# Performance work log

Hardware: AMD Instinct MI355X
Metric: run time of the kernel (lower is better)

Reference implementation:

```python
import jax, jax.numpy as jnp
import numpy as np

N = 100000        # num nodes
E = 1200000       # num edges (avg degree 12)
F_IN = 64         # num_features
HID = 64          # hidden_size
NCLS = 40         # num_classes
K = 2             # propagation hops


def setup_inputs() -> dict:
    key = jax.random.key(0)
    k0, k1, k2, k3 = jax.random.split(key, 4)
    x = jax.random.normal(k0, (N, F_IN), dtype=jnp.float32)
    edge_index = jax.random.randint(k1, (2, E), 0, N, dtype=jnp.int32)
    # SGConv's internal Linear (in->hidden) and the classifier fc (hidden->classes)
    W1 = jax.random.normal(k2, (F_IN, HID), dtype=jnp.float32) / np.sqrt(F_IN).astype(np.float32)
    b1 = jnp.zeros((HID,), jnp.float32)
    W2 = jax.random.normal(k3, (HID, NCLS), dtype=jnp.float32) / np.sqrt(HID).astype(np.float32)
    b2 = jnp.zeros((NCLS,), jnp.float32)
    return {"x": x, "edge_index": edge_index, "W1": W1, "b1": b1, "W2": W2, "b2": b2}


def reference(x, edge_index, W1, b1, W2, b2):
    n = x.shape[0]
    # gcn_norm: add self-loops with weight 1, symmetric normalization
    loop = jnp.arange(n, dtype=edge_index.dtype)
    src = jnp.concatenate([edge_index[0], loop])  # message source j
    dst = jnp.concatenate([edge_index[1], loop])  # aggregation target i
    deg = jax.ops.segment_sum(jnp.ones(src.shape, x.dtype), dst, num_segments=n)
    dinv = jnp.where(deg > 0, jax.lax.rsqrt(deg), 0.0)
    norm = dinv[src] * dinv[dst]  # [E+N]
    # K-hop propagation: x_i <- sum_j norm_ij * x_j
    for _ in range(K):
        x = jax.ops.segment_sum(norm[:, None] * x[src], dst, num_segments=n)
    h = jax.nn.relu(x @ W1 + b1)          # SGConv lin + ReLU
    logits = h @ W2 + b2                  # fc
    return jax.nn.log_softmax(logits, axis=1)
```

## Files before the change

kernel.cpp:

```cpp
#include <hip/hip_runtime.h>
#include <math.h>

#define N_NODES 100000
#define BSHIFT 9
#define NBUCK 256

typedef unsigned short bfu;
typedef unsigned int uint;
typedef __attribute__((ext_vector_type(8))) short short8v;
typedef __attribute__((ext_vector_type(4))) float f32x4;

__device__ __forceinline__ float bf2f(bfu u) {
    union { uint i; float f; } v; v.i = (uint)u << 16; return v.f;
}
__device__ __forceinline__ bfu f2bf(float f) {
    union { float f_; uint i; } v; v.f_ = f;
    uint r = (v.i + 0x7FFFu + ((v.i >> 16) & 1u)) >> 16;
    return (bfu)r;
}

__global__ __launch_bounds__(256) void bucket_hist(const int* __restrict__ dst,
                                                   int* __restrict__ gcount, int nE) {
    __shared__ int h[NBUCK];
    int tid = threadIdx.x;
    h[tid] = 0;
    __syncthreads();
    for (int e = blockIdx.x * 256 + tid; e < nE; e += gridDim.x * 256)
        atomicAdd(&h[dst[e] >> BSHIFT], 1);
    __syncthreads();
    if (h[tid]) atomicAdd(&gcount[tid], h[tid]);
}

__global__ __launch_bounds__(NBUCK) void scan_buckets(const int* __restrict__ gcount,
                                                      int* __restrict__ gbase,
                                                      int* __restrict__ gcursor) {
    __shared__ int s[NBUCK];
    int t = threadIdx.x;
    int v = gcount[t];
    s[t] = v;
    __syncthreads();
    #pragma unroll
    for (int off = 1; off < NBUCK; off <<= 1) {
        int tv = (t >= off) ? s[t - off] : 0;
        __syncthreads();
        s[t] += tv;
        __syncthreads();
    }
    gbase[t] = s[t] - v;
    gcursor[t] = s[t] - v;
}

__global__ __launch_bounds__(256) void bin_edges(const int* __restrict__ src,
                                                 const int* __restrict__ dst,
                                                 int* __restrict__ gcursor,
                                                 uint* __restrict__ binned, int nE) {
    __shared__ int h[NBUCK];
    __shared__ int base[NBUCK];
    int tid = threadIdx.x;
    int start = blockIdx.x * 4096;
    h[tid] = 0;
    __syncthreads();
    int bkt[16], rnk[16];
    #pragma unroll
    for (int u = 0; u < 16; ++u) {
        int e = start + u * 256 + tid;
        bkt[u] = -1;
        if (e < nE) {
            int b = dst[e] >> BSHIFT;
            bkt[u] = b;
            rnk[u] = atomicAdd(&h[b], 1);
        }
    }
    __syncthreads();
    base[tid] = h[tid] ? atomicAdd(&gcursor[tid], h[tid]) : 0;
    __syncthreads();
    #pragma unroll
    for (int u = 0; u < 16; ++u) {
        int e = start + u * 256 + tid;
        if (e < nE) {
            uint pk = ((uint)(dst[e] & 511) << 17) | (uint)src[e];
            binned[base[bkt[u]] + rnk[u]] = pk;
        }
    }
}

__global__ __launch_bounds__(512) void build_csr(
    const uint* __restrict__ binned, const int* __restrict__ gbase,
    const int* __restrict__ gcount, int* __restrict__ rowptr,
    float* __restrict__ dinv, int* __restrict__ nbr, int nN, int nE) {
    __shared__ int hist[512];
    __shared__ int cursor[512];
    int b = blockIdx.x, t = threadIdx.x;
    int n0 = b << BSHIFT;
    int nNodes = min(512, nN - n0);
    int base = gbase[b], cnt = gcount[b];
    hist[t] = 0;
    __syncthreads();
    for (int i = t; i < cnt; i += 512)
        atomicAdd(&hist[binned[base + i] >> 17], 1);
    __syncthreads();
    int v = hist[t];
    #pragma unroll
    for (int off = 1; off < 512; off <<= 1) {
        int tv = (t >= off) ? hist[t - off] : 0;
        __syncthreads();
        hist[t] += tv;
        __syncthreads();
    }
    int excl = hist[t] - v;
    if (t < nNodes) {
        rowptr[n0 + t] = base + excl;
        dinv[n0 + t] = rsqrtf((float)v + 1.0f);
    }
    cursor[t] = excl;
    __syncthreads();
    for (int i = t; i < cnt; i += 512) {
        uint pk = binned[base + i];
        int ld = pk >> 17;
        int pos = atomicAdd(&cursor[ld], 1);
        nbr[base + pos] = (int)(pk & 0x1FFFFu);
    }
    if (b == 0 && t == 0) rowptr[nN] = nE;
}

__global__ void scale_to_bf16(ushort4* __restrict__ z0, const float4* __restrict__ x,
                              const float* __restrict__ dinv, int n4) {
    int t = blockIdx.x * blockDim.x + threadIdx.x;
    if (t >= n4) return;
    float w = dinv[t >> 4];
    float4 v = x[t];
    ushort4 o;
    o.x = f2bf(w * v.x); o.y = f2bf(w * v.y);
    o.z = f2bf(w * v.z); o.w = f2bf(w * v.w);
    z0[t] = o;
}

template<int PW>
__global__ __launch_bounds__(256) void gather_hop8(
    bfu* __restrict__ out, const bfu* __restrict__ z,
    const int* __restrict__ nbr, const int* __restrict__ rowptr,
    const float* __restrict__ dinv, int nN) {
    int node = blockIdx.x * 4 + (threadIdx.x >> 6);
    if (node >= nN) return;
    int lane = threadIdx.x & 63;
    int g = lane >> 3, k = lane & 7;
    int beg = rowptr[node], end = rowptr[node + 1];

    float acc[8];
    #pragma unroll
    for (int i = 0; i < 8; ++i) acc[i] = 0.f;

    auto accum = [&](uint4 v) {
        union { uint u; float f; } t;
        t.u = v.x << 16;         acc[0] += t.f;
        t.u = v.x & 0xFFFF0000u; acc[1] += t.f;
        t.u = v.y << 16;         acc[2] += t.f;
        t.u = v.y & 0xFFFF0000u; acc[3] += t.f;
        t.u = v.z << 16;         acc[4] += t.f;
        t.u = v.z & 0xFFFF0000u; acc[5] += t.f;
        t.u = v.w << 16;         acc[6] += t.f;
        t.u = v.w & 0xFFFF0000u; acc[7] += t.f;
    };

    if (g == 0)
        accum(reinterpret_cast<const uint4*>(z + (size_t)node * 64)[k]);
    for (int j = beg + g; j < end; j += 8)
        accum(reinterpret_cast<const uint4*>(z + (size_t)nbr[j] * 64)[k]);

    #pragma unroll
    for (int m = 8; m < 64; m <<= 1)
        #pragma unroll
        for (int i = 0; i < 8; ++i)
            acc[i] += __shfl_xor(acc[i], m);

    if (g == 0) {
        float di = dinv[node];
        float w = (PW == 2) ? di * di : di;
        uint4 o;
        o.x = ((uint)f2bf(acc[1] * w) << 16) | f2bf(acc[0] * w);
        o.y = ((uint)f2bf(acc[3] * w) << 16) | f2bf(acc[2] * w);
        o.z = ((uint)f2bf(acc[5] * w) << 16) | f2bf(acc[4] * w);
        o.w = ((uint)f2bf(acc[7] * w) << 16) | f2bf(acc[6] * w);
        reinterpret_cast<uint4*>(out + (size_t)node * 64)[k] = o;
    }
}

__global__ __launch_bounds__(256) void mlp_mfma(
    float* __restrict__ out, const bfu* __restrict__ zC,
    const float* __restrict__ W1, const float* __restrict__ b1,
    const float* __restrict__ W2, const float* __restrict__ b2, int nN) {
    __shared__ short w1t[64 * 72];
    __shared__ short w2t[48 * 72];
    __shared__ short hlds[64 * 72];
    __shared__ float b1s[64];
    __shared__ float b2s[48];

    int tid = threadIdx.x;
    for (int i = tid; i < 64 * 64; i += 256) {
        int k = i >> 6, n = i & 63;
        w1t[n * 72 + k] = (short)f2bf(W1[i]);
    }
    for (int i = tid; i < 48 * 64; i += 256) {
        int k = i / 48, n = i % 48;
        w2t[n * 72 + k] = (short)(n < 40 ? f2bf(W2[k * 40 + n]) : 0);
    }
    if (tid < 64) b1s[tid] = b1[tid];
    if (tid >= 64 && tid < 112) b2s[tid - 64] = (tid - 64 < 40) ? b2[tid - 64] : 0.f;

    int wv = tid >> 6, l = tid & 63;
    int li = l & 15, kg = l >> 4;
    int nodebase = blockIdx.x * 64 + wv * 16;
    int nclamp = min(nodebase + li, nN - 1);

    const short8v* zr = (const short8v*)(zC + (size_t)nclamp * 64);
    short8v a0 = zr[kg];
    short8v a1 = zr[kg + 4];
    __syncthreads();

    f32x4 acc[4];
    #pragma unroll
    for (int nt = 0; nt < 4; ++nt) {
        f32x4 c = {0.f, 0.f, 0.f, 0.f};
        short8v b0 = *(const short8v*)&w1t[(nt * 16 + li) * 72 + kg * 8];
        short8v b1f = *(const short8v*)&w1t[(nt * 16 + li) * 72 + 32 + kg * 8];
        c = __builtin_amdgcn_mfma_f32_16x16x32_bf16(a0, b0, c, 0, 0, 0);
        c = __builtin_amdgcn_mfma_f32_16x16x32_bf16(a1, b1f, c, 0, 0, 0);
        acc[nt] = c;
    }
    #pragma unroll
    for (int nt = 0; nt < 4; ++nt) {
        float bb = b1s[nt * 16 + li];
        #pragma unroll
        for (int r = 0; r < 4; ++r) {
            float v = fmaxf(acc[nt][r] + bb, 0.f);
            hlds[(wv * 16 + kg * 4 + r) * 72 + nt * 16 + li] = (short)f2bf(v);
        }
    }
    __syncthreads();

    const short8v* hp = (const short8v*)&hlds[(wv * 16 + li) * 72];
    short8v ha0 = hp[kg];
    short8v ha1 = hp[kg + 4];
    f32x4 acc2[3];
    #pragma unroll
    for (int nt = 0; nt < 3; ++nt) {
        f32x4 c = {0.f, 0.f, 0.f, 0.f};
        short8v b0 = *(const short8v*)&w2t[(nt * 16 + li) * 72 + kg * 8];
        short8v b1f = *(const short8v*)&w2t[(nt * 16 + li) * 72 + 32 + kg * 8];
        c = __builtin_amdgcn_mfma_f32_16x16x32_bf16(ha0, b0, c, 0, 0, 0);
        c = __builtin_amdgcn_mfma_f32_16x16x32_bf16(ha1, b1f, c, 0, 0, 0);
        acc2[nt] = c;
    }

    float lg[3][4];
    #pragma unroll
    for (int nt = 0; nt < 3; ++nt) {
        float bb = b2s[nt * 16 + li];
        #pragma unroll
        for (int r = 0; r < 4; ++r) lg[nt][r] = acc2[nt][r] + bb;
    }
    bool v2 = (li < 8);
    float mx[4], sm[4];
    #pragma unroll
    for (int r = 0; r < 4; ++r) {
        float m = fmaxf(lg[0][r], lg[1][r]);
        if (v2) m = fmaxf(m, lg[2][r]);
        mx[r] = m;
    }
    #pragma unroll
    for (int off = 1; off < 16; off <<= 1)
        #pragma unroll
        for (int r = 0; r < 4; ++r)
            mx[r] = fmaxf(mx[r], __shfl_xor(mx[r], off));
    #pragma unroll
    for (int r = 0; r < 4; ++r) {
        float s = expf(lg[0][r] - mx[r]) + expf(lg[1][r] - mx[r]);
        if (v2) s += expf(lg[2][r] - mx[r]);
        sm[r] = s;
    }
    #pragma unroll
    for (int off = 1; off < 16; off <<= 1)
        #pragma unroll
        for (int r = 0; r < 4; ++r)
            sm[r] += __shfl_xor(sm[r], off);

    int nb2 = nodebase + kg * 4;
    #pragma unroll
    for (int r = 0; r < 4; ++r) {
        int nd = nb2 + r;
        if (nd < nN) {
            float lse = mx[r] + logf(sm[r]);
            out[(size_t)nd * 40 + li]      = lg[0][r] - lse;
            out[(size_t)nd * 40 + 16 + li] = lg[1][r] - lse;
            if (v2) out[(size_t)nd * 40 + 32 + li] = lg[2][r] - lse;
        }
    }
}

extern "C" void kernel_launch(void* const* d_in, const int* in_sizes, int n_in,
                              void* d_out, int out_size, void* d_ws, size_t ws_size,
                              hipStream_t stream) {
    const float* x   = (const float*)d_in[0];
    const int* eidx  = (const int*)d_in[1];
    const float* W1  = (const float*)d_in[2];
    const float* b1  = (const float*)d_in[3];
    const float* W2  = (const float*)d_in[4];
    const float* b2  = (const float*)d_in[5];
    float* out = (float*)d_out;

    const int nN = N_NODES;
    const int nE = in_sizes[1] / 2;
    const int* src = eidx;
    const int* dst = eidx + nE;
    const int nBk = (nN + 511) >> BSHIFT;

    char* ws = (char*)d_ws;
    size_t off = 0;
    auto alloc = [&](size_t bytes) {
        char* p = ws + off;
        off += (bytes + 255) & ~(size_t)255;
        return p;
    };
    float* dinv    = (float*)alloc((size_t)nN * 4);
    int*   gcount  = (int*)  alloc(NBUCK * 4);
    int*   gbase   = (int*)  alloc(NBUCK * 4);
    int*   gcursor = (int*)  alloc(NBUCK * 4);
    int*   rowptr  = (int*)  alloc((size_t)(nN + 1) * 4);
    uint*  binned  = (uint*) alloc((size_t)nE * 4);
    int*   nbr     = (int*)  alloc((size_t)nE * 4);
    bfu*   z0      = (bfu*)  alloc((size_t)nN * 64 * 2);
    bfu*   zB      = (bfu*)  alloc((size_t)nN * 64 * 2);
    bfu*   zC      = (bfu*)  alloc((size_t)nN * 64 * 2);

    hipMemsetAsync(gcount, 0, NBUCK * 4, stream);
    bucket_hist<<<640, 256, 0, stream>>>(dst, gcount, nE);
    scan_buckets<<<1, NBUCK, 0, stream>>>(gcount, gbase, gcursor);
    bin_edges<<<(nE + 4095) / 4096, 256, 0, stream>>>(src, dst, gcursor, binned, nE);
    build_csr<<<nBk, 512, 0, stream>>>(binned, gbase, gcount, rowptr, dinv, nbr, nN, nE);

    const int n4 = nN * 16;
    scale_to_bf16<<<(n4 + 255) / 256, 256, 0, stream>>>((ushort4*)z0, (const float4*)x, dinv, n4);
    const int gBlocks = (nN + 3) / 4;
    gather_hop8<2><<<gBlocks, 256, 0, stream>>>(zB, z0, nbr, rowptr, dinv, nN);
    gather_hop8<1><<<gBlocks, 256, 0, stream>>>(zC, zB, nbr, rowptr, dinv, nN);

    mlp_mfma<<<(nN + 63) / 64, 256, 0, stream>>>(out, zC, W1, b1, W2, b2, nN);
}
```

Measured before the change: 166.0 us.

## Fuse bf16 feature scaling into CSR build and unroll neighbor gather by two

```diff
diff --git a/kernel.cpp b/kernel.cpp
--- a/kernel.cpp
+++ b/kernel.cpp
@@ -87,7 +87,8 @@
 __global__ __launch_bounds__(512) void build_csr(
     const uint* __restrict__ binned, const int* __restrict__ gbase,
     const int* __restrict__ gcount, int* __restrict__ rowptr,
-    float* __restrict__ dinv, int* __restrict__ nbr, int nN, int nE) {
+    float* __restrict__ dinv, int* __restrict__ nbr,
+    const float4* __restrict__ x, ushort4* __restrict__ z0, int nN, int nE) {
     __shared__ int hist[512];
     __shared__ int cursor[512];
     int b = blockIdx.x, t = threadIdx.x;
@@ -108,11 +109,13 @@
         __syncthreads();
     }
     int excl = hist[t] - v;
+    float dv = rsqrtf((float)v + 1.0f);
     if (t < nNodes) {
         rowptr[n0 + t] = base + excl;
-        dinv[n0 + t] = rsqrtf((float)v + 1.0f);
+        dinv[n0 + t] = dv;
     }
     cursor[t] = excl;
+    ((float*)hist)[t] = dv;
     __syncthreads();
     for (int i = t; i < cnt; i += 512) {
         uint pk = binned[base + i];
@@ -120,23 +123,22 @@
         int pos = atomicAdd(&cursor[ld], 1);
         nbr[base + pos] = (int)(pk & 0x1FFFFu);
     }
+    const float4* xr = x + (size_t)n0 * 16;
+    ushort4* zr = z0 + (size_t)n0 * 16;
+    int totalF4 = nNodes * 16;
+    for (int i = t; i < totalF4; i += 512) {
+        float w = ((float*)hist)[i >> 4];
+        float4 vv = xr[i];
+        ushort4 o;
+        o.x = f2bf(w * vv.x); o.y = f2bf(w * vv.y);
+        o.z = f2bf(w * vv.z); o.w = f2bf(w * vv.w);
+        zr[i] = o;
+    }
     if (b == 0 && t == 0) rowptr[nN] = nE;
 }
 
-__global__ void scale_to_bf16(ushort4* __restrict__ z0, const float4* __restrict__ x,
-                              const float* __restrict__ dinv, int n4) {
-    int t = blockIdx.x * blockDim.x + threadIdx.x;
-    if (t >= n4) return;
-    float w = dinv[t >> 4];
-    float4 v = x[t];
-    ushort4 o;
-    o.x = f2bf(w * v.x); o.y = f2bf(w * v.y);
-    o.z = f2bf(w * v.z); o.w = f2bf(w * v.w);
-    z0[t] = o;
-}
-
 template<int PW>
-__global__ __launch_bounds__(256) void gather_hop8(
+__global__ __launch_bounds__(256, 8) void gather_hop8(
     bfu* __restrict__ out, const bfu* __restrict__ z,
     const int* __restrict__ nbr, const int* __restrict__ rowptr,
     const float* __restrict__ dinv, int nN) {
@@ -150,6 +152,9 @@
     #pragma unroll
     for (int i = 0; i < 8; ++i) acc[i] = 0.f;
 
+    auto rowload = [&](int s) -> uint4 {
+        return reinterpret_cast<const uint4*>(z + (size_t)s * 64)[k];
+    };
     auto accum = [&](uint4 v) {
         union { uint u; float f; } t;
         t.u = v.x << 16;         acc[0] += t.f;
@@ -163,9 +168,17 @@
     };
 
     if (g == 0)
-        accum(reinterpret_cast<const uint4*>(z + (size_t)node * 64)[k]);
-    for (int j = beg + g; j < end; j += 8)
-        accum(reinterpret_cast<const uint4*>(z + (size_t)nbr[j] * 64)[k]);
+        accum(rowload(node));
+    int j = beg + g;
+    for (; j + 8 < end; j += 16) {
+        int i0 = nbr[j], i1 = nbr[j + 8];
+        uint4 v0 = rowload(i0);
+        uint4 v1 = rowload(i1);
+        accum(v0);
+        accum(v1);
+    }
+    if (j < end)
+        accum(rowload(nbr[j]));
 
     #pragma unroll
     for (int m = 8; m < 64; m <<= 1)
@@ -336,10 +349,9 @@
     bucket_hist<<<640, 256, 0, stream>>>(dst, gcount, nE);
     scan_buckets<<<1, NBUCK, 0, stream>>>(gcount, gbase, gcursor);
     bin_edges<<<(nE + 4095) / 4096, 256, 0, stream>>>(src, dst, gcursor, binned, nE);
-    build_csr<<<nBk, 512, 0, stream>>>(binned, gbase, gcount, rowptr, dinv, nbr, nN, nE);
-
-    const int n4 = nN * 16;
-    scale_to_bf16<<<(n4 + 255) / 256, 256, 0, stream>>>((ushort4*)z0, (const float4*)x, dinv, n4);
+    build_csr<<<nBk, 512, 0, stream>>>(binned, gbase, gcount, rowptr, dinv, nbr,
+                                       (const float4*)x, (ushort4*)z0, nN, nE);
+
     const int gBlocks = (nN + 3) / 4;
     gather_hop8<2><<<gBlocks, 256, 0, stream>>>(zB, z0, nbr, rowptr, dinv, nN);
     gather_hop8<1><<<gBlocks, 256, 0, stream>>>(zC, zB, nbr, rowptr, dinv, nN);
```

Result: faster. 162.2 us (-2.3%).
